# Kernel tuning notes

Hardware: AMD Instinct MI355X
Metric: run time of the kernel (lower is better)

## Reference

```python
import jax, jax.numpy as jnp
import numpy as np

B, P, C, H, W = 32, 6, 2048, 16, 8   # batch, parts-per-image, feat_dim, feature map
HEADS, DHEAD, LAYERS = 4, 512, 2      # GATv2: hidden = feat_dim // heads
N = B * P                             # graph nodes


def setup_inputs() -> dict:
    key = jax.random.key(0)
    ks = jax.random.split(key, 6)
    return {
        "features": jax.random.normal(ks[0], (B, P * C, H, W), jnp.float32),
        "img_num_ps": jax.random.randint(ks[1], (B,), 1, P + 1, jnp.int32),
        "Wl": jax.random.normal(ks[2], (LAYERS, HEADS, C, DHEAD), jnp.float32) * 0.02,
        "bl": jnp.zeros((LAYERS, HEADS, DHEAD), jnp.float32),
        "Wr": jax.random.normal(ks[3], (LAYERS, HEADS, C, DHEAD), jnp.float32) * 0.02,
        "br": jnp.zeros((LAYERS, HEADS, DHEAD), jnp.float32),
        "att": jax.random.normal(ks[4], (LAYERS, HEADS, DHEAD), jnp.float32) * 0.05,
        "gat_bias": jnp.zeros((LAYERS, HEADS * DHEAD), jnp.float32),
        "bn_gamma": jnp.ones((C,), jnp.float32),
        "bn_mean": jnp.zeros((C,), jnp.float32),
        "bn_var": jnp.ones((C,), jnp.float32),
    }


def _intra_mask(img_num_ps):
    # instance one-hot (blocks of 6) + one_hot_refine zeroing, then adj = oh @ oh.T == 1
    node = jnp.arange(N)
    valid = (node % P) < img_num_ps[node // P]
    inst = node // P
    adj = (inst[:, None] == inst[None, :]) & valid[:, None] & valid[None, :]
    # PyG GATv2Conv: remove existing self loops then add self loops for all nodes
    return adj | jnp.eye(N, dtype=bool)


def _gatv2(x, mask, Wl, bl, Wr, br, att, gat_bias):
    NEG = jnp.float32(-1e30)
    for l in range(LAYERS):
        xl = jnp.einsum('nc,hcd->nhd', x, Wl[l]) + bl[l]  # source (lin_l)
        xr = jnp.einsum('nc,hcd->nhd', x, Wr[l]) + br[l]  # target (lin_r)
        z = jax.nn.leaky_relu(xr[:, None] + xl[None, :], 0.2)   # [i,j,h,d]
        s = jnp.einsum('ijhd,hd->hij', z, att[l])               # [h,i,j]
        s = jnp.where(mask[None], s, NEG)
        alpha = jax.nn.softmax(s, axis=-1)                      # softmax over sources j
        out = jnp.einsum('hij,jhd->ihd', alpha, xl)
        x = out.reshape(N, HEADS * DHEAD) + gat_bias[l]
        if l < LAYERS - 1:
            x = jax.nn.elu(x)
    return x


def reference(features, img_num_ps, Wl, bl, Wr, br, att, gat_bias, bn_gamma, bn_mean, bn_var):
    # torch.chunk(features, 6, dim=1) -> cat(dim=0): chunk-major node ordering
    parts = features.reshape(B, P, C, H, W).transpose(1, 0, 2, 3, 4).reshape(N, C, H, W)
    pool_feat = parts.mean(axis=(2, 3))                     # GlobalAvgPool -> [N, C]
    mask = _intra_mask(img_num_ps)
    graph_feat = _gatv2(pool_feat, mask, Wl, bl, Wr, br, att, gat_bias) + pool_feat
    # chunk(graph_feat, 6, dim=0) stacked on dim=1, mean over parts -> [B, C]
    gfa = graph_feat.reshape(P, B, C).transpose(1, 0, 2).mean(axis=1)
    # BN neck, eval mode, frozen bias = 0
    return bn_gamma * (gfa - bn_mean) / jnp.sqrt(bn_var + 1e-5)
```

## Files before the change

kernel.cpp:

```cpp
#include <hip/hip_runtime.h>
#include <hip/hip_bf16.h>


#define NNODES 192
#define CFEAT  2048

typedef __attribute__((ext_vector_type(8))) short bf16x8;
typedef __attribute__((ext_vector_type(4))) float f32x4;

__device__ inline unsigned f2bf(float f) {
    union { float f; unsigned u; } v; v.f = f;
    unsigned u = v.u;
    u += 0x7FFFu + ((u >> 16) & 1u);
    return u >> 16;
}

__global__ __launch_bounds__(256) void pool_kernel(const float* __restrict__ F,
                                                   float* __restrict__ POOL,
                                                   unsigned short* __restrict__ POOLB) {
    int wave = threadIdx.x >> 6, lane = threadIdx.x & 63;
    #pragma unroll
    for (int it = 0; it < 12; ++it) {
        int dr = blockIdx.x * 4 + wave + it * 16384;
        int r0 = dr * 2;
        int n = r0 >> 11, c0 = r0 & 2047;
        int p = n >> 5, b = n & 31;
        const float* src = F + (((size_t)b * 12288 + (size_t)p * 2048 + c0) << 7);
        float4 v = *(const float4*)(src + (lane << 2));
        float acc = (v.x + v.y) + (v.z + v.w);
        acc += __shfl_down(acc, 16);
        acc += __shfl_down(acc, 8);
        acc += __shfl_down(acc, 4);
        acc += __shfl_down(acc, 2);
        acc += __shfl_down(acc, 1);
        if ((lane & 31) == 0) {
            int r = r0 + (lane >> 5);
            float m = acc * (1.0f / 128.0f);
            POOL[r] = m;
            POOLB[r] = (unsigned short)f2bf(m);
        }
    }
}

__global__ __launch_bounds__(256) void gemm_kernel(
    const unsigned short* __restrict__ X,
    const float* __restrict__ WL,
    const float* __restrict__ WR,
    float* __restrict__ P) {
    __shared__ unsigned short lA[192 * 40];
    __shared__ unsigned short lB[32 * 40];

    int ct = blockIdx.x, sk = blockIdx.y;
    const float* Wb = (ct >= 64 ? WR : WL)
                    + (size_t)((ct & 63) >> 4) * (2048 * 512) + ((ct & 15) << 5);
    int kbeg = sk << 8;
    int t = threadIdx.x, w = t >> 6, l = t & 63;
    int rA = t >> 2, qA = t & 3;
    int colB = t & 31, kgB = t >> 5;

    f32x4 acc[3][2];
    #pragma unroll
    for (int i = 0; i < 3; ++i)
        #pragma unroll
        for (int j = 0; j < 2; ++j) acc[i][j] = {0.f, 0.f, 0.f, 0.f};

    uint4 av0, av1, av2;
    float bv0, bv1, bv2, bv3;
    {
        const unsigned short* xp = X + (size_t)rA * 2048 + kbeg + qA * 8;
        av0 = *(const uint4*)(xp);
        av1 = *(const uint4*)(xp + 64 * 2048);
        av2 = *(const uint4*)(xp + 128 * 2048);
        const float* wp = Wb + (size_t)(kbeg + kgB * 4) * 512 + colB;
        bv0 = wp[0]; bv1 = wp[512]; bv2 = wp[1024]; bv3 = wp[1536];
    }

    for (int step = 0; step < 8; ++step) {
        __syncthreads();
        *(uint4*)(lA + rA * 40 + qA * 8) = av0;
        *(uint4*)(lA + (rA + 64) * 40 + qA * 8) = av1;
        *(uint4*)(lA + (rA + 128) * 40 + qA * 8) = av2;
        uint2 bw;
        bw.x = f2bf(bv0) | (f2bf(bv1) << 16);
        bw.y = f2bf(bv2) | (f2bf(bv3) << 16);
        *(uint2*)(lB + colB * 40 + kgB * 4) = bw;
        __syncthreads();

        if (step < 7) {
            int k0 = kbeg + ((step + 1) << 5);
            const unsigned short* xp = X + (size_t)rA * 2048 + k0 + qA * 8;
            av0 = *(const uint4*)(xp);
            av1 = *(const uint4*)(xp + 64 * 2048);
            av2 = *(const uint4*)(xp + 128 * 2048);
            const float* wp = Wb + (size_t)(k0 + kgB * 4) * 512 + colB;
            bv0 = wp[0]; bv1 = wp[512]; bv2 = wp[1024]; bv3 = wp[1536];
        }

        int lr = l & 15, lk = (l >> 4) << 3;
        bf16x8 af0 = *(const bf16x8*)(lA + (48 * w + lr) * 40 + lk);
        bf16x8 af1 = *(const bf16x8*)(lA + (48 * w + 16 + lr) * 40 + lk);
        bf16x8 af2 = *(const bf16x8*)(lA + (48 * w + 32 + lr) * 40 + lk);
        bf16x8 bf0 = *(const bf16x8*)(lB + lr * 40 + lk);
        bf16x8 bf1 = *(const bf16x8*)(lB + (16 + lr) * 40 + lk);
        acc[0][0] = __builtin_amdgcn_mfma_f32_16x16x32_bf16(af0, bf0, acc[0][0], 0, 0, 0);
        acc[0][1] = __builtin_amdgcn_mfma_f32_16x16x32_bf16(af0, bf1, acc[0][1], 0, 0, 0);
        acc[1][0] = __builtin_amdgcn_mfma_f32_16x16x32_bf16(af1, bf0, acc[1][0], 0, 0, 0);
        acc[1][1] = __builtin_amdgcn_mfma_f32_16x16x32_bf16(af1, bf1, acc[1][1], 0, 0, 0);
        acc[2][0] = __builtin_amdgcn_mfma_f32_16x16x32_bf16(af2, bf0, acc[2][0], 0, 0, 0);
        acc[2][1] = __builtin_amdgcn_mfma_f32_16x16x32_bf16(af2, bf1, acc[2][1], 0, 0, 0);
    }

    float* Pb = P + (size_t)sk * (192 * 4096) + (ct << 5);
    #pragma unroll
    for (int fi = 0; fi < 3; ++fi) {
        int rbase = 48 * w + 16 * fi + ((l >> 4) << 2);
        #pragma unroll
        for (int j = 0; j < 4; ++j) {
            float* dst = Pb + (size_t)(rbase + j) * 4096 + (l & 15);
            dst[0]  = acc[fi][0][j];
            dst[16] = acc[fi][1][j];
        }
    }
}

template <int LAYER>
__global__ __launch_bounds__(256) void attn_kernel(
    const float* __restrict__ P,
    const float* __restrict__ BL,
    const float* __restrict__ BR,
    const float* __restrict__ ATT,
    const float* __restrict__ GBIAS,
    const int* __restrict__ NPS,
    const float* __restrict__ POOL,
    float* __restrict__ OUTF,
    unsigned short* __restrict__ OUTB) {
    __shared__ float xls[6][512];
    __shared__ float xrs[6][512];
    __shared__ float atts[512];
    __shared__ float s_sm[6][6];
    __shared__ float alpha[6][6];

    int g = blockIdx.x, h = blockIdx.y;
    int tid = threadIdx.x;
    int cnt = NPS[g];

    for (int idx = tid; idx < 6 * 512; idx += 256) {
        int q = idx >> 9, d = idx & 511;
        int col = h * 512 + d;
        size_t base = (size_t)(g * 6 + q) * 4096 + col;
        float sl = BL[col], sr = BR[col];
        #pragma unroll
        for (int sk = 0; sk < 8; ++sk) {
            const float* Ps = P + (size_t)sk * (192 * 4096) + base;
            sl += Ps[0];
            sr += Ps[2048];
        }
        xls[q][d] = sl;
        xrs[q][d] = sr;
    }
    for (int d = tid; d < 512; d += 256) atts[d] = ATT[h * 512 + d];
    __syncthreads();

    int wv = tid >> 6, lane = tid & 63;
    for (int p = wv; p < 36; p += 4) {
        int i = p / 6, j = p % 6;
        float acc = 0.f;
        #pragma unroll
        for (int u = 0; u < 8; ++u) {
            int d = lane + u * 64;
            float v = xrs[i][d] + xls[j][d];
            v = (v >= 0.f) ? v : 0.2f * v;
            acc = fmaf(atts[d], v, acc);
        }
        #pragma unroll
        for (int off = 32; off; off >>= 1) acc += __shfl_down(acc, off);
        if (lane == 0) s_sm[i][j] = acc;
    }
    __syncthreads();

    if (tid < 6) {
        int i = tid;
        bool iv = i < cnt;
        float mx;
        if (iv) {
            mx = -1e30f;
            for (int j = 0; j < cnt; ++j) mx = fmaxf(mx, s_sm[i][j]);
        } else {
            mx = s_sm[i][i];
        }
        float e[6], sum = 0.f;
        for (int j = 0; j < 6; ++j) {
            bool nb = iv ? (j < cnt) : (j == i);
            e[j] = nb ? expf(s_sm[i][j] - mx) : 0.f;
            sum += e[j];
        }
        float inv = 1.f / sum;
        for (int j = 0; j < 6; ++j) alpha[i][j] = e[j] * inv;
    }
    __syncthreads();

    for (int idx = tid; idx < 6 * 512; idx += 256) {
        int q = idx >> 9, d = idx & 511;
        float acc = 0.f;
        #pragma unroll
        for (int j = 0; j < 6; ++j) acc = fmaf(alpha[q][j], xls[j][d], acc);
        int col = h * 512 + d;
        size_t off = (size_t)(g * 6 + q) * 2048 + col;
        float v = acc + GBIAS[col];
        if (LAYER == 0) {
            v = (v > 0.f) ? v : expm1f(v);
            OUTB[off] = (unsigned short)f2bf(v);
        } else {
            OUTF[off] = v + POOL[off];
        }
    }
}

__global__ __launch_bounds__(256) void final_kernel(
    const float* __restrict__ GF, const float* __restrict__ GAMMA,
    const float* __restrict__ MEAN, const float* __restrict__ VAR,
    float* __restrict__ OUTP) {
    int idx = blockIdx.x * 256 + threadIdx.x;
    int c = idx & 2047, b = idx >> 11;
    float acc = 0.f;
    #pragma unroll
    for (int p = 0; p < 6; ++p) acc += GF[(size_t)(p * 32 + b) * 2048 + c];
    acc *= (1.f / 6.f);
    OUTP[idx] = GAMMA[c] * (acc - MEAN[c]) * rsqrtf(VAR[c] + 1e-5f);
}

extern "C" void kernel_launch(void* const* d_in, const int* in_sizes, int n_in,
                              void* d_out, int out_size, void* d_ws, size_t ws_size,
                              hipStream_t stream) {
    const float* F     = (const float*)d_in[0];
    const int*   nps   = (const int*)d_in[1];
    const float* Wl    = (const float*)d_in[2];
    const float* bl    = (const float*)d_in[3];
    const float* Wr    = (const float*)d_in[4];
    const float* br    = (const float*)d_in[5];
    const float* att   = (const float*)d_in[6];
    const float* gb    = (const float*)d_in[7];
    const float* gamma = (const float*)d_in[8];
    const float* mean  = (const float*)d_in[9];
    const float* var   = (const float*)d_in[10];
    float* out = (float*)d_out;
    float* wsf = (float*)d_ws;

    const size_t SZ = (size_t)NNODES * CFEAT;
    float* pool = wsf;
    float* gf   = wsf + SZ;
    float* P    = wsf + 2 * SZ;
    unsigned short* poolb = (unsigned short*)(wsf + 18 * SZ);
    unsigned short* x1b   = poolb + SZ;

    const size_t WOFF = 4ull * 2048 * 512;

    pool_kernel<<<dim3(4096), dim3(256), 0, stream>>>(F, pool, poolb);

    gemm_kernel<<<dim3(128, 8), dim3(256), 0, stream>>>(poolb, Wl, Wr, P);
    attn_kernel<0><<<dim3(32, 4), dim3(256), 0, stream>>>(P, bl, br, att, gb, nps,
                                                          nullptr, nullptr, x1b);

    gemm_kernel<<<dim3(128, 8), dim3(256), 0, stream>>>(x1b, Wl + WOFF, Wr + WOFF, P);
    attn_kernel<1><<<dim3(32, 4), dim3(256), 0, stream>>>(P, bl + 2048, br + 2048,
                                                          att + 2048, gb + 2048,
                                                          nps, pool, gf, nullptr);

    final_kernel<<<dim3(256), dim3(256), 0, stream>>>(gf, gamma, mean, var, out);
}
```

Baseline: 123.0 us.

## Drop LDS staging in projection GEMM and store split-K partials as bf16

Measured after the change: 148.3 us. 1.21x slower.

```diff
diff --git a/kernel.cpp b/kernel.cpp
--- a/kernel.cpp
+++ b/kernel.cpp
@@ -13,6 +13,10 @@
     unsigned u = v.u;
     u += 0x7FFFu + ((u >> 16) & 1u);
     return u >> 16;
+}
+__device__ inline float bf2f(unsigned short u) {
+    union { unsigned u; float f; } v; v.u = (unsigned)u << 16;
+    return v.f;
 }
 
 __global__ __launch_bounds__(256) void pool_kernel(const float* __restrict__ F,
@@ -46,86 +50,51 @@
     const unsigned short* __restrict__ X,
     const float* __restrict__ WL,
     const float* __restrict__ WR,
-    float* __restrict__ P) {
-    __shared__ unsigned short lA[192 * 40];
-    __shared__ unsigned short lB[32 * 40];
-
-    int ct = blockIdx.x, sk = blockIdx.y;
-    const float* Wb = (ct >= 64 ? WR : WL)
-                    + (size_t)((ct & 63) >> 4) * (2048 * 512) + ((ct & 15) << 5);
+    unsigned short* __restrict__ P) {
+    int bx = blockIdx.x, sk = blockIdx.y;
+    int t = threadIdx.x, w = t >> 6, l = t & 63;
+    int lr = l & 15, lg = l >> 4;
     int kbeg = sk << 8;
-    int t = threadIdx.x, w = t >> 6, l = t & 63;
-    int rA = t >> 2, qA = t & 3;
-    int colB = t & 31, kgB = t >> 5;
-
-    f32x4 acc[3][2];
-    #pragma unroll
-    for (int i = 0; i < 3; ++i)
-        #pragma unroll
-        for (int j = 0; j < 2; ++j) acc[i][j] = {0.f, 0.f, 0.f, 0.f};
-
-    uint4 av0, av1, av2;
-    float bv0, bv1, bv2, bv3;
-    {
-        const unsigned short* xp = X + (size_t)rA * 2048 + kbeg + qA * 8;
-        av0 = *(const uint4*)(xp);
-        av1 = *(const uint4*)(xp + 64 * 2048);
-        av2 = *(const uint4*)(xp + 128 * 2048);
-        const float* wp = Wb + (size_t)(kbeg + kgB * 4) * 512 + colB;
-        bv0 = wp[0]; bv1 = wp[512]; bv2 = wp[1024]; bv3 = wp[1536];
-    }
+
+    const float* Wb = (bx >= 32 ? WR : WL)
+                    + (size_t)((bx & 31) >> 3) * (2048 * 512)
+                    + ((bx & 7) << 6) + (w << 4) + lr;
+    const unsigned short* Xp = X + (size_t)lr * 2048 + kbeg + lg * 8;
+
+    f32x4 acc[12];
+    #pragma unroll
+    for (int i = 0; i < 12; ++i) acc[i] = {0.f, 0.f, 0.f, 0.f};
 
     for (int step = 0; step < 8; ++step) {
-        __syncthreads();
-        *(uint4*)(lA + rA * 40 + qA * 8) = av0;
-        *(uint4*)(lA + (rA + 64) * 40 + qA * 8) = av1;
-        *(uint4*)(lA + (rA + 128) * 40 + qA * 8) = av2;
-        uint2 bw;
-        bw.x = f2bf(bv0) | (f2bf(bv1) << 16);
-        bw.y = f2bf(bv2) | (f2bf(bv3) << 16);
-        *(uint2*)(lB + colB * 40 + kgB * 4) = bw;
-        __syncthreads();
-
-        if (step < 7) {
-            int k0 = kbeg + ((step + 1) << 5);
-            const unsigned short* xp = X + (size_t)rA * 2048 + k0 + qA * 8;
-            av0 = *(const uint4*)(xp);
-            av1 = *(const uint4*)(xp + 64 * 2048);
-            av2 = *(const uint4*)(xp + 128 * 2048);
-            const float* wp = Wb + (size_t)(k0 + kgB * 4) * 512 + colB;
-            bv0 = wp[0]; bv1 = wp[512]; bv2 = wp[1024]; bv3 = wp[1536];
-        }
-
-        int lr = l & 15, lk = (l >> 4) << 3;
-        bf16x8 af0 = *(const bf16x8*)(lA + (48 * w + lr) * 40 + lk);
-        bf16x8 af1 = *(const bf16x8*)(lA + (48 * w + 16 + lr) * 40 + lk);
-        bf16x8 af2 = *(const bf16x8*)(lA + (48 * w + 32 + lr) * 40 + lk);
-        bf16x8 bf0 = *(const bf16x8*)(lB + lr * 40 + lk);
-        bf16x8 bf1 = *(const bf16x8*)(lB + (16 + lr) * 40 + lk);
-        acc[0][0] = __builtin_amdgcn_mfma_f32_16x16x32_bf16(af0, bf0, acc[0][0], 0, 0, 0);
-        acc[0][1] = __builtin_amdgcn_mfma_f32_16x16x32_bf16(af0, bf1, acc[0][1], 0, 0, 0);
-        acc[1][0] = __builtin_amdgcn_mfma_f32_16x16x32_bf16(af1, bf0, acc[1][0], 0, 0, 0);
-        acc[1][1] = __builtin_amdgcn_mfma_f32_16x16x32_bf16(af1, bf1, acc[1][1], 0, 0, 0);
-        acc[2][0] = __builtin_amdgcn_mfma_f32_16x16x32_bf16(af2, bf0, acc[2][0], 0, 0, 0);
-        acc[2][1] = __builtin_amdgcn_mfma_f32_16x16x32_bf16(af2, bf1, acc[2][1], 0, 0, 0);
-    }
-
-    float* Pb = P + (size_t)sk * (192 * 4096) + (ct << 5);
-    #pragma unroll
-    for (int fi = 0; fi < 3; ++fi) {
-        int rbase = 48 * w + 16 * fi + ((l >> 4) << 2);
-        #pragma unroll
-        for (int j = 0; j < 4; ++j) {
-            float* dst = Pb + (size_t)(rbase + j) * 4096 + (l & 15);
-            dst[0]  = acc[fi][0][j];
-            dst[16] = acc[fi][1][j];
-        }
-    }
+        int k0 = step << 5;
+        const float* wp = Wb + (size_t)(kbeg + k0 + lg * 8) * 512;
+        float b0 = wp[0],        b1 = wp[512],      b2 = wp[2 * 512], b3 = wp[3 * 512];
+        float b4 = wp[4 * 512],  b5 = wp[5 * 512],  b6 = wp[6 * 512], b7 = wp[7 * 512];
+        uint4 bb;
+        bb.x = f2bf(b0) | (f2bf(b1) << 16);
+        bb.y = f2bf(b2) | (f2bf(b3) << 16);
+        bb.z = f2bf(b4) | (f2bf(b5) << 16);
+        bb.w = f2bf(b6) | (f2bf(b7) << 16);
+        bf16x8 bfr = __builtin_bit_cast(bf16x8, bb);
+        #pragma unroll
+        for (int fi = 0; fi < 12; ++fi) {
+            bf16x8 af = *(const bf16x8*)(Xp + (size_t)fi * 16 * 2048 + k0);
+            acc[fi] = __builtin_amdgcn_mfma_f32_16x16x32_bf16(af, bfr, acc[fi], 0, 0, 0);
+        }
+    }
+
+    unsigned short* Pp = P + (size_t)sk * (192 * 4096)
+                       + (size_t)(lg * 4) * 4096 + (bx << 6) + (w << 4) + lr;
+    #pragma unroll
+    for (int fi = 0; fi < 12; ++fi)
+        #pragma unroll
+        for (int j = 0; j < 4; ++j)
+            Pp[(size_t)(fi * 16 + j) * 4096] = (unsigned short)f2bf(acc[fi][j]);
 }
 
 template <int LAYER>
 __global__ __launch_bounds__(256) void attn_kernel(
-    const float* __restrict__ P,
+    const unsigned short* __restrict__ P,
     const float* __restrict__ BL,
     const float* __restrict__ BR,
     const float* __restrict__ ATT,
@@ -151,9 +120,9 @@
         float sl = BL[col], sr = BR[col];
         #pragma unroll
         for (int sk = 0; sk < 8; ++sk) {
-            const float* Ps = P + (size_t)sk * (192 * 4096) + base;
-            sl += Ps[0];
-            sr += Ps[2048];
+            const unsigned short* Ps = P + (size_t)sk * (192 * 4096) + base;
+            sl += bf2f(Ps[0]);
+            sr += bf2f(Ps[2048]);
         }
         xls[q][d] = sl;
         xrs[q][d] = sr;
@@ -249,19 +218,19 @@
     const size_t SZ = (size_t)NNODES * CFEAT;
     float* pool = wsf;
     float* gf   = wsf + SZ;
-    float* P    = wsf + 2 * SZ;
-    unsigned short* poolb = (unsigned short*)(wsf + 18 * SZ);
-    unsigned short* x1b   = poolb + SZ;
+    unsigned short* P     = (unsigned short*)(wsf + 2 * SZ);
+    unsigned short* poolb = (unsigned short*)(wsf + 10 * SZ);
+    unsigned short* x1b   = (unsigned short*)(wsf + 11 * SZ);
 
     const size_t WOFF = 4ull * 2048 * 512;
 
     pool_kernel<<<dim3(4096), dim3(256), 0, stream>>>(F, pool, poolb);
 
-    gemm_kernel<<<dim3(128, 8), dim3(256), 0, stream>>>(poolb, Wl, Wr, P);
+    gemm_kernel<<<dim3(64, 8), dim3(256), 0, stream>>>(poolb, Wl, Wr, P);
     attn_kernel<0><<<dim3(32, 4), dim3(256), 0, stream>>>(P, bl, br, att, gb, nps,
                                                           nullptr, nullptr, x1b);
 
-    gemm_kernel<<<dim3(128, 8), dim3(256), 0, stream>>>(x1b, Wl + WOFF, Wr + WOFF, P);
+    gemm_kernel<<<dim3(64, 8), dim3(256), 0, stream>>>(x1b, Wl + WOFF, Wr + WOFF, P);
     attn_kernel<1><<<dim3(32, 4), dim3(256), 0, stream>>>(P, bl + 2048, br + 2048,
                                                           att + 2048, gb + 2048,
                                                           nps, pool, gf, nullptr);
```
